# Kernel tuning notes

Hardware: AMD Instinct MI355X
Metric: run time of the kernel (lower is better)

The kernel has to match this reference:

```python
import jax, jax.numpy as jnp
from jax import lax
import numpy as np

LRELU_SLOPE = 0.1
DILATIONS = (1, 2, 4)
B, C, T = 8, 256, 8192


def pd_indexing(x, d, dilation):
    """Pitch-dependent past/future gather along time.
    x: (B, C, T); d: (B, 1, T) float dilation factors.
    Returns xP, xF: (B, C, T), zero where index is out of range.
    """
    b, c, t_len = x.shape
    t = jnp.arange(t_len, dtype=x.dtype)  # (T,)
    dil = d[:, 0, :] * dilation           # (B, T)
    idxP = jnp.round(t[None, :] - dil).astype(jnp.int32)  # (B, T)
    idxF = jnp.round(t[None, :] + dil).astype(jnp.int32)  # (B, T)
    validP = (idxP >= 0).astype(x.dtype)[:, None, :]        # (B,1,T)
    validF = (idxF < t_len).astype(x.dtype)[:, None, :]
    idxPc = jnp.broadcast_to(jnp.clip(idxP, 0, t_len - 1)[:, None, :], (b, c, t_len))
    idxFc = jnp.broadcast_to(jnp.clip(idxF, 0, t_len - 1)[:, None, :], (b, c, t_len))
    xP = jnp.take_along_axis(x, idxPc, axis=2) * validP
    xF = jnp.take_along_axis(x, idxFc, axis=2) * validF
    return xP, xF


def conv1x1(x, w, bias):
    # x: (B,C,T), w: (O,C), bias: (O,)
    return jnp.einsum('oc,bct->bot', w, x) + bias[None, :, None]


def conv3(x, w, bias):
    # x: (B,C,T), w: (O,C,3), padding=1
    y = lax.conv_general_dilated(x, w, window_strides=(1,), padding=[(1, 1)],
                                 dimension_numbers=('NCH', 'OIH', 'NCH'))
    return y + bias[None, :, None]


def setup_inputs() -> dict:
    key = jax.random.key(0)
    ks = jax.random.split(key, 8)
    x = jax.random.normal(ks[0], (B, C, T), dtype=jnp.float32)
    d = jax.random.uniform(ks[1], (B, 1, T), dtype=jnp.float32, minval=0.0, maxval=16.0)
    n = len(DILATIONS)
    s1 = 1.0 / np.sqrt(C)
    s3 = 1.0 / np.sqrt(3 * C)
    WC = jax.random.normal(ks[2], (n, C, C), dtype=jnp.float32) * s1
    WP = jax.random.normal(ks[3], (n, C, C), dtype=jnp.float32) * s1
    WF = jax.random.normal(ks[4], (n, C, C), dtype=jnp.float32) * s1
    WA = jax.random.normal(ks[5], (n, C, C, 3), dtype=jnp.float32) * s3
    bC = jnp.zeros((n, C), dtype=jnp.float32)
    bP = jnp.zeros((n, C), dtype=jnp.float32)
    bF = jnp.zeros((n, C), dtype=jnp.float32)
    bA = jnp.zeros((n, C), dtype=jnp.float32)
    return {"x": x, "d": d, "WC": WC, "bC": bC, "WP": WP, "bP": bP,
            "WF": WF, "bF": bF, "WA": WA, "bA": bA}


def reference(x, d, WC, bC, WP, bP, WF, bF, WA, bA):
    for i, dilation in enumerate(DILATIONS):
        xt = jax.nn.leaky_relu(x, LRELU_SLOPE)
        xP, xF = pd_indexing(xt, d, dilation)
        xt = conv1x1(xt, WC[i], bC[i]) + conv1x1(xP, WP[i], bP[i]) + conv1x1(xF, WF[i], bF[i])
        xt = jax.nn.leaky_relu(xt, LRELU_SLOPE)
        xt = conv3(xt, WA[i], bA[i])
        x = xt + x
    return x
```

## Files before the change

### kernel.cpp

```cpp
#include <hip/hip_runtime.h>
#include <hip/hip_bf16.h>
#include <cstddef>
#include <cstdint>

constexpr int Bn = 8, Cn = 256, Tn = 8192;
constexpr int NL = 3;
constexpr int Kc = 768;
constexpr float SLOPE = 0.1f;

typedef unsigned short u16;
using bf8   = __attribute__((ext_vector_type(8))) short;
using f32x4 = __attribute__((ext_vector_type(4))) float;

__device__ __forceinline__ float lrelu(float v) { return v > 0.f ? v : SLOPE * v; }
__device__ __forceinline__ u16 f2bf(float f) {
    __hip_bfloat16 h = __float2bfloat16(f);
    return *reinterpret_cast<u16*>(&h);
}

__device__ __forceinline__ void g2l16(const u16* g, u16* l) {
    __builtin_amdgcn_global_load_lds(
        (const __attribute__((address_space(1))) char*)g,
        (__attribute__((address_space(3))) char*)l, 16, 0, 0);
}

__device__ __forceinline__ void pipe_barrier() {
    __builtin_amdgcn_s_barrier();
    __builtin_amdgcn_sched_barrier(0);
}

__global__ __launch_bounds__(256)
void k_wprep(const float* __restrict__ WC, const float* __restrict__ WP,
             const float* __restrict__ WF, const float* __restrict__ WA,
             const float* __restrict__ bC, const float* __restrict__ bP,
             const float* __restrict__ bF,
             u16* __restrict__ Wcat, u16* __restrict__ WAp, float* __restrict__ bSum,
             u16* __restrict__ zrow)
{
    if (blockIdx.x == 0) zrow[threadIdx.x] = 0;
    const int n1 = NL * Cn * Kc;
    for (int i = blockIdx.x * blockDim.x + threadIdx.x; i < n1;
         i += gridDim.x * blockDim.x) {
        int c = i % Cn;
        int s = (i / Cn) % 3;
        int o = (i / (3 * Cn)) % Cn;
        int l = i / (3 * Cn * Cn);
        size_t src = ((size_t)l * Cn + o) * Cn + c;
        float wc = (s == 0) ? WC[src] : (s == 1) ? WP[src] : WF[src];
        Wcat[i] = f2bf(wc);
        WAp[i] = f2bf(WA[src * 3 + s]);
    }
    for (int i = blockIdx.x * blockDim.x + threadIdx.x; i < NL * Cn;
         i += gridDim.x * blockDim.x)
        bSum[i] = bC[i] + bP[i] + bF[i];
}

__global__ __launch_bounds__(256)
void k_prep(const float* __restrict__ x, u16* __restrict__ xT)
{
    __shared__ float s[64][65];
    const int b = blockIdx.z, c0 = blockIdx.y * 64, t0 = blockIdx.x * 64;
    const int tid = threadIdx.x;
    const float* xb = x + ((size_t)b * Cn + c0) * Tn + t0;

    int tt = tid & 63, c4 = tid >> 6;
    for (int cc = c4; cc < 64; cc += 4)
        s[cc][tt] = xb[(size_t)cc * Tn + tt];
    __syncthreads();

    int ccS = tid & 63, t4 = tid >> 6;
    u16* xTb = xT + ((size_t)b * Tn + t0) * Cn + c0;
    for (int t2 = t4; t2 < 64; t2 += 4)
        xTb[(size_t)t2 * Cn + ccS] = f2bf(lrelu(s[ccS][t2]));
}

__global__ __launch_bounds__(256, 2)
void k_gemm1(const u16* __restrict__ xT, const float* __restrict__ d,
             const u16* __restrict__ Wl, const float* __restrict__ bS,
             float dil, u16* __restrict__ zT, const u16* __restrict__ zrow)
{
    __shared__ u16 smem[8 * 4096];
    __shared__ int sRow[3][128];

    const int tid = threadIdx.x;
    const int b = blockIdx.z;
    const int fid = blockIdx.x;
    const int j = fid >> 3;
    const int o0 = (j & 1) * 128;
    const int t0 = ((fid & 7) * 8 + (j >> 1)) * 128;

    if (tid < 128) {
        int t = t0 + tid;
        float dv = d[(size_t)b * Tn + t] * dil;
        int ip = (int)rintf((float)t - dv);
        int iF = (int)rintf((float)t + dv);
        sRow[0][tid] = t;
        sRow[1][tid] = (ip >= 0) ? ip : -1;
        sRow[2][tid] = (iF < Tn) ? iF : -1;
    }
    __syncthreads();

    const int srow = tid >> 2;
    const int schunkL = (tid & 3) * 8;
    const int schunkG = ((tid & 3) ^ ((tid >> 3) & 3)) * 8;
    const u16* xTb = xT + (size_t)b * Tn * Cn;

    const u16 *pr0[3], *pr1[3];
    #pragma unroll
    for (int s = 0; s < 3; ++s) {
        int r0 = sRow[s][srow], r1 = sRow[s][srow + 64];
        pr0[s] = (r0 >= 0) ? (xTb + (size_t)r0 * Cn + schunkG) : (zrow + schunkG);
        pr1[s] = (r1 >= 0) ? (xTb + (size_t)r1 * Cn + schunkG) : (zrow + schunkG);
    }
    const u16* wbase = Wl + (size_t)(o0 + srow) * Kc + schunkG;

    const int lane = tid & 63, wv = tid >> 6;
    const int wm = (wv & 1) * 64;
    const int wn = (wv >> 1) * 64;
    const int lr = lane & 15, quad = lane >> 4;
    const int rchunk = (quad ^ ((lr >> 1) & 3)) * 8;

    const int ldsW = srow * 32 + schunkL;
    const int ldsW2 = (srow + 64) * 32 + schunkL;

    auto dma = [&](int kg, int bsel) {
        int seg = kg >> 3, kk = (kg & 7) * 32;
        u16* bx = smem + bsel * 4096;
        u16* bw = smem + 16384 + bsel * 4096;
        g2l16(wbase + seg * 256 + kk,                   bw + ldsW);
        g2l16(wbase + (size_t)64 * Kc + seg * 256 + kk, bw + ldsW2);
        g2l16(pr0[seg] + kk, bx + ldsW);
        g2l16(pr1[seg] + kk, bx + ldsW2);
    };

    f32x4 acc[4][4] = {};
    dma(0, 0); dma(1, 1);

    #pragma unroll
    for (int P = 0; P < 12; ++P) {
        const int k0 = 2 * P, k1 = 2 * P + 1;
        asm volatile("s_waitcnt vmcnt(0) lgkmcnt(0)" ::: "memory");
        pipe_barrier();
        if (P < 11) { dma(k0 + 2, (k0 + 2) & 3); dma(k1 + 2, (k1 + 2) & 3); }
        __builtin_amdgcn_sched_barrier(0);

        const u16* bX0 = smem + (k0 & 3) * 4096;
        const u16* bW0 = smem + 16384 + (k0 & 3) * 4096;
        const u16* bX1 = smem + (k1 & 3) * 4096;
        const u16* bW1 = smem + 16384 + (k1 & 3) * 4096;

        bf8 a0[4], g0[4], a1[4], g1[4];
        #pragma unroll
        for (int mi = 0; mi < 4; ++mi)
            a0[mi] = *(const bf8*)(bX0 + (wm + mi * 16 + lr) * 32 + rchunk);
        #pragma unroll
        for (int ni = 0; ni < 4; ++ni)
            g0[ni] = *(const bf8*)(bW0 + (wn + ni * 16 + lr) * 32 + rchunk);
        __builtin_amdgcn_sched_barrier(0);
        #pragma unroll
        for (int mi = 0; mi < 4; ++mi)
            a1[mi] = *(const bf8*)(bX1 + (wm + mi * 16 + lr) * 32 + rchunk);
        #pragma unroll
        for (int ni = 0; ni < 4; ++ni)
            g1[ni] = *(const bf8*)(bW1 + (wn + ni * 16 + lr) * 32 + rchunk);

        asm volatile("s_waitcnt lgkmcnt(8)" ::: "memory");
        __builtin_amdgcn_sched_barrier(0);
        __builtin_amdgcn_s_setprio(1);
        #pragma unroll
        for (int mi = 0; mi < 4; ++mi)
            #pragma unroll
            for (int ni = 0; ni < 4; ++ni)
                acc[mi][ni] = __builtin_amdgcn_mfma_f32_16x16x32_bf16(
                    a0[mi], g0[ni], acc[mi][ni], 0, 0, 0);
        __builtin_amdgcn_s_setprio(0);

        asm volatile("s_waitcnt lgkmcnt(0)" ::: "memory");
        __builtin_amdgcn_sched_barrier(0);
        __builtin_amdgcn_s_setprio(1);
        #pragma unroll
        for (int mi = 0; mi < 4; ++mi)
            #pragma unroll
            for (int ni = 0; ni < 4; ++ni)
                acc[mi][ni] = __builtin_amdgcn_mfma_f32_16x16x32_bf16(
                    a1[mi], g1[ni], acc[mi][ni], 0, 0, 0);
        __builtin_amdgcn_s_setprio(0);
    }

    float bias[4];
    #pragma unroll
    for (int ni = 0; ni < 4; ++ni) bias[ni] = bS[o0 + wn + ni * 16 + lr];
    u16* zTb = zT + (size_t)b * Tn * Cn;
    #pragma unroll
    for (int mi = 0; mi < 4; ++mi)
        #pragma unroll
        for (int r = 0; r < 4; ++r) {
            int t = t0 + wm + mi * 16 + quad * 4 + r;
            u16* row = zTb + (size_t)t * Cn + o0 + wn;
            #pragma unroll
            for (int ni = 0; ni < 4; ++ni)
                row[ni * 16 + lr] = f2bf(lrelu(acc[mi][ni][r] + bias[ni]));
        }
}

__global__ __launch_bounds__(256, 2)
void k_gemm2(const u16* __restrict__ zT, const u16* __restrict__ WAl,
             const float* __restrict__ bA, const float* __restrict__ xres,
             float* __restrict__ out, u16* __restrict__ xTn, int writeXT,
             const u16* __restrict__ zrow)
{
    __shared__ u16 smem[8 * 4096];

    const int tid = threadIdx.x;
    const int b = blockIdx.z;
    const int fid = blockIdx.x;
    const int j = fid >> 3;
    const int o0 = (j & 1) * 128;
    const int t0 = ((fid & 7) * 8 + (j >> 1)) * 128;

    const int srow = tid >> 2;
    const int schunkL = (tid & 3) * 8;
    const int schunkG = ((tid & 3) ^ ((tid >> 3) & 3)) * 8;
    const int lane = tid & 63, wv = tid >> 6;
    const int wo = (wv & 1) * 64;
    const int wt = (wv >> 1) * 64;
    const int lr = lane & 15, quad = lane >> 4;
    const int rchunk = (quad ^ ((lr >> 1) & 3)) * 8;

    const u16* zTb = zT + (size_t)b * Tn * Cn;
    const u16 *zr0[3], *zr1[3];
    #pragma unroll
    for (int tap = 0; tap < 3; ++tap) {
        int r0 = t0 + srow + tap - 1;
        int r1 = r0 + 64;
        zr0[tap] = (r0 >= 0 && r0 < Tn) ? (zTb + (size_t)r0 * Cn + schunkG)
                                        : (zrow + schunkG);
        zr1[tap] = (r1 >= 0 && r1 < Tn) ? (zTb + (size_t)r1 * Cn + schunkG)
                                        : (zrow + schunkG);
    }
    const u16* wbase = WAl + (size_t)(o0 + srow) * Kc + schunkG;

    const int ldsW = srow * 32 + schunkL;
    const int ldsW2 = (srow + 64) * 32 + schunkL;

    auto dma = [&](int kg, int bsel) {
        int tap = kg >> 3, kk = (kg & 7) * 32;
        u16* bz = smem + bsel * 4096;
        u16* bw = smem + 16384 + bsel * 4096;
        g2l16(wbase + tap * 256 + kk,                   bw + ldsW);
        g2l16(wbase + (size_t)64 * Kc + tap * 256 + kk, bw + ldsW2);
        g2l16(zr0[tap] + kk, bz + ldsW);
        g2l16(zr1[tap] + kk, bz + ldsW2);
    };

    f32x4 acc[4][4] = {};
    dma(0, 0); dma(1, 1);

    #pragma unroll
    for (int P = 0; P < 12; ++P) {
        const int k0 = 2 * P, k1 = 2 * P + 1;
        asm volatile("s_waitcnt vmcnt(0) lgkmcnt(0)" ::: "memory");
        pipe_barrier();
        if (P < 11) { dma(k0 + 2, (k0 + 2) & 3); dma(k1 + 2, (k1 + 2) & 3); }
        __builtin_amdgcn_sched_barrier(0);

        const u16* bZ0 = smem + (k0 & 3) * 4096;
        const u16* bW0 = smem + 16384 + (k0 & 3) * 4096;
        const u16* bZ1 = smem + (k1 & 3) * 4096;
        const u16* bW1 = smem + 16384 + (k1 & 3) * 4096;

        bf8 a0[4], g0[4], a1[4], g1[4];
        #pragma unroll
        for (int mi = 0; mi < 4; ++mi)
            a0[mi] = *(const bf8*)(bW0 + (wo + mi * 16 + lr) * 32 + rchunk);
        #pragma unroll
        for (int ni = 0; ni < 4; ++ni)
            g0[ni] = *(const bf8*)(bZ0 + (wt + ni * 16 + lr) * 32 + rchunk);
        __builtin_amdgcn_sched_barrier(0);
        #pragma unroll
        for (int mi = 0; mi < 4; ++mi)
            a1[mi] = *(const bf8*)(bW1 + (wo + mi * 16 + lr) * 32 + rchunk);
        #pragma unroll
        for (int ni = 0; ni < 4; ++ni)
            g1[ni] = *(const bf8*)(bZ1 + (wt + ni * 16 + lr) * 32 + rchunk);

        asm volatile("s_waitcnt lgkmcnt(8)" ::: "memory");
        __builtin_amdgcn_sched_barrier(0);
        __builtin_amdgcn_s_setprio(1);
        #pragma unroll
        for (int mi = 0; mi < 4; ++mi)
            #pragma unroll
            for (int ni = 0; ni < 4; ++ni)
                acc[mi][ni] = __builtin_amdgcn_mfma_f32_16x16x32_bf16(
                    a0[mi], g0[ni], acc[mi][ni], 0, 0, 0);
        __builtin_amdgcn_s_setprio(0);

        asm volatile("s_waitcnt lgkmcnt(0)" ::: "memory");
        __builtin_amdgcn_sched_barrier(0);
        __builtin_amdgcn_s_setprio(1);
        #pragma unroll
        for (int mi = 0; mi < 4; ++mi)
            #pragma unroll
            for (int ni = 0; ni < 4; ++ni)
                acc[mi][ni] = __builtin_amdgcn_mfma_f32_16x16x32_bf16(
                    a1[mi], g1[ni], acc[mi][ni], 0, 0, 0);
        __builtin_amdgcn_s_setprio(0);
    }

    float biasv[4][4];
    #pragma unroll
    for (int mi = 0; mi < 4; ++mi) {
        float4 bb = *(const float4*)(bA + o0 + wo + mi * 16 + quad * 4);
        biasv[mi][0] = bb.x; biasv[mi][1] = bb.y; biasv[mi][2] = bb.z; biasv[mi][3] = bb.w;
    }

    float xr0[16], xr1[16];
    ushort4 pkv[4][4];
    auto issue = [&](int ni, float* dst) {
        #pragma unroll
        for (int mi = 0; mi < 4; ++mi)
            #pragma unroll
            for (int r = 0; r < 4; ++r) {
                int o = o0 + wo + mi * 16 + quad * 4 + r;
                dst[mi * 4 + r] =
                    xres[((size_t)b * Cn + o) * Tn + t0 + wt + ni * 16 + lr];
            }
    };
    issue(0, xr0);
    #pragma unroll
    for (int ni = 0; ni < 4; ++ni) {
        float* cur = (ni & 1) ? xr1 : xr0;
        float* nxt = (ni & 1) ? xr0 : xr1;
        if (ni + 1 < 4) issue(ni + 1, nxt);
        #pragma unroll
        for (int mi = 0; mi < 4; ++mi) {
            ushort4 pk;
            #pragma unroll
            for (int r = 0; r < 4; ++r) {
                int o = o0 + wo + mi * 16 + quad * 4 + r;
                size_t idx = ((size_t)b * Cn + o) * Tn + t0 + wt + ni * 16 + lr;
                float v = acc[mi][ni][r] + biasv[mi][r] + cur[mi * 4 + r];
                out[idx] = v;
                ((u16*)&pk)[r] = f2bf(lrelu(v));
            }
            pkv[ni][mi] = pk;
        }
    }

    if (writeXT) {
        u16* strip = smem + wv * 1152;
        u16* xTb2 = xTn + (size_t)b * Tn * Cn;
        #pragma unroll
        for (int ni = 0; ni < 4; ++ni) {
            __syncthreads();
            #pragma unroll
            for (int mi = 0; mi < 4; ++mi)
                *(ushort4*)(strip + lr * 72 + mi * 16 + quad * 4) = pkv[ni][mi];
            __syncthreads();
            #pragma unroll
            for (int it = 0; it < 2; ++it) {
                int tt = (lane >> 3) + it * 8;
                uint4 vv = *(const uint4*)(strip + tt * 72 + (lane & 7) * 8);
                *(uint4*)(xTb2 + (size_t)(t0 + wt + ni * 16 + tt) * Cn
                          + o0 + wo + (lane & 7) * 8) = vv;
            }
        }
    }
}

extern "C" void kernel_launch(void* const* d_in, const int* in_sizes, int n_in,
                              void* d_out, int out_size, void* d_ws, size_t ws_size,
                              hipStream_t stream)
{
    const float* x  = (const float*)d_in[0];
    const float* d  = (const float*)d_in[1];
    const float* WC = (const float*)d_in[2];
    const float* bC = (const float*)d_in[3];
    const float* WP = (const float*)d_in[4];
    const float* bP = (const float*)d_in[5];
    const float* WF = (const float*)d_in[6];
    const float* bF = (const float*)d_in[7];
    const float* WA = (const float*)d_in[8];
    const float* bA = (const float*)d_in[9];
    float* out = (float*)d_out;

    char* ws = (char*)d_ws;
    u16*   xT   = (u16*)(ws);
    u16*   zT   = (u16*)(ws + (size_t)Bn * Tn * Cn * 2);
    u16*   Wcat = (u16*)(ws + (size_t)2 * Bn * Tn * Cn * 2);
    u16*   WAp  = Wcat + (size_t)NL * Cn * Kc;
    float* bSum = (float*)(WAp + (size_t)NL * Cn * Kc);
    u16*   zrow = (u16*)(bSum + NL * Cn);

    k_wprep<<<dim3(1024), dim3(256), 0, stream>>>(WC, WP, WF, WA, bC, bP, bF,
                                                  Wcat, WAp, bSum, zrow);

    dim3 gP(Tn / 64, Cn / 64, Bn);
    dim3 gG(128, 1, Bn);
    dim3 blk(256);

    k_prep<<<gP, blk, 0, stream>>>(x, xT);

    const float dils[NL] = {1.f, 2.f, 4.f};
    const float* xcur = x;
    for (int i = 0; i < NL; ++i) {
        k_gemm1<<<gG, blk, 0, stream>>>(xT, d,
                                        Wcat + (size_t)i * Cn * Kc,
                                        bSum + (size_t)i * Cn,
                                        dils[i], zT, zrow);
        k_gemm2<<<gG, blk, 0, stream>>>(zT,
                                        WAp + (size_t)i * Cn * Kc,
                                        bA + (size_t)i * Cn,
                                        xcur, out, xT, (i < NL - 1) ? 1 : 0,
                                        zrow);
        xcur = out;
    }
}
```

Before: 364.0 us.

## Loop each block over both output halves, coalesce zT stores, prefetch residual

Both GEMM kernels now assign one time tile per block and loop over the two 128-channel output halves inside the block, so the grid shrinks from 128 to 64 blocks per batch. The first GEMM now stages its bf16 epilogue through a per-wave LDS strip, so zT is written with 16-byte row stores instead of scattered 2-byte stores. The second GEMM loads half of the residual values before the main loop and drops the block-wide barriers from its per-wave transpose. In exchange, the two halves run back to back inside each block, and the smaller grid gives the GPU fewer blocks to spread across compute units.

```diff
diff --git a/kernel.cpp b/kernel.cpp
--- a/kernel.cpp
+++ b/kernel.cpp
@@ -85,9 +85,7 @@
     const int tid = threadIdx.x;
     const int b = blockIdx.z;
     const int fid = blockIdx.x;
-    const int j = fid >> 3;
-    const int o0 = (j & 1) * 128;
-    const int t0 = ((fid & 7) * 8 + (j >> 1)) * 128;
+    const int t0 = ((fid & 7) * 8 + (fid >> 3)) * 128;
 
     if (tid < 128) {
         int t = t0 + tid;
@@ -112,7 +110,6 @@
         pr0[s] = (r0 >= 0) ? (xTb + (size_t)r0 * Cn + schunkG) : (zrow + schunkG);
         pr1[s] = (r1 >= 0) ? (xTb + (size_t)r1 * Cn + schunkG) : (zrow + schunkG);
     }
-    const u16* wbase = Wl + (size_t)(o0 + srow) * Kc + schunkG;
 
     const int lane = tid & 63, wv = tid >> 6;
     const int wm = (wv & 1) * 64;
@@ -122,85 +119,102 @@
 
     const int ldsW = srow * 32 + schunkL;
     const int ldsW2 = (srow + 64) * 32 + schunkL;
-
-    auto dma = [&](int kg, int bsel) {
-        int seg = kg >> 3, kk = (kg & 7) * 32;
-        u16* bx = smem + bsel * 4096;
-        u16* bw = smem + 16384 + bsel * 4096;
-        g2l16(wbase + seg * 256 + kk,                   bw + ldsW);
-        g2l16(wbase + (size_t)64 * Kc + seg * 256 + kk, bw + ldsW2);
-        g2l16(pr0[seg] + kk, bx + ldsW);
-        g2l16(pr1[seg] + kk, bx + ldsW2);
-    };
-
-    f32x4 acc[4][4] = {};
-    dma(0, 0); dma(1, 1);
-
-    #pragma unroll
-    for (int P = 0; P < 12; ++P) {
-        const int k0 = 2 * P, k1 = 2 * P + 1;
-        asm volatile("s_waitcnt vmcnt(0) lgkmcnt(0)" ::: "memory");
-        pipe_barrier();
-        if (P < 11) { dma(k0 + 2, (k0 + 2) & 3); dma(k1 + 2, (k1 + 2) & 3); }
-        __builtin_amdgcn_sched_barrier(0);
-
-        const u16* bX0 = smem + (k0 & 3) * 4096;
-        const u16* bW0 = smem + 16384 + (k0 & 3) * 4096;
-        const u16* bX1 = smem + (k1 & 3) * 4096;
-        const u16* bW1 = smem + 16384 + (k1 & 3) * 4096;
-
-        bf8 a0[4], g0[4], a1[4], g1[4];
-        #pragma unroll
-        for (int mi = 0; mi < 4; ++mi)
-            a0[mi] = *(const bf8*)(bX0 + (wm + mi * 16 + lr) * 32 + rchunk);
-        #pragma unroll
-        for (int ni = 0; ni < 4; ++ni)
-            g0[ni] = *(const bf8*)(bW0 + (wn + ni * 16 + lr) * 32 + rchunk);
-        __builtin_amdgcn_sched_barrier(0);
-        #pragma unroll
-        for (int mi = 0; mi < 4; ++mi)
-            a1[mi] = *(const bf8*)(bX1 + (wm + mi * 16 + lr) * 32 + rchunk);
-        #pragma unroll
-        for (int ni = 0; ni < 4; ++ni)
-            g1[ni] = *(const bf8*)(bW1 + (wn + ni * 16 + lr) * 32 + rchunk);
-
-        asm volatile("s_waitcnt lgkmcnt(8)" ::: "memory");
-        __builtin_amdgcn_sched_barrier(0);
-        __builtin_amdgcn_s_setprio(1);
-        #pragma unroll
-        for (int mi = 0; mi < 4; ++mi)
+    u16* zTb = zT + (size_t)b * Tn * Cn;
+
+    #pragma unroll 1
+    for (int h = 0; h < 2; ++h) {
+        const int o0 = h * 128;
+        if (h) __syncthreads();
+
+        const u16* wbase = Wl + (size_t)(o0 + srow) * Kc + schunkG;
+        auto dma = [&](int kg, int bsel) {
+            int seg = kg >> 3, kk = (kg & 7) * 32;
+            u16* bx = smem + bsel * 4096;
+            u16* bw = smem + 16384 + bsel * 4096;
+            g2l16(wbase + seg * 256 + kk,                   bw + ldsW);
+            g2l16(wbase + (size_t)64 * Kc + seg * 256 + kk, bw + ldsW2);
+            g2l16(pr0[seg] + kk, bx + ldsW);
+            g2l16(pr1[seg] + kk, bx + ldsW2);
+        };
+
+        float bias[4];
+        #pragma unroll
+        for (int ni = 0; ni < 4; ++ni) bias[ni] = bS[o0 + wn + ni * 16 + lr];
+
+        f32x4 acc[4][4] = {};
+        dma(0, 0); dma(1, 1);
+
+        #pragma unroll
+        for (int P = 0; P < 12; ++P) {
+            const int k0 = 2 * P, k1 = 2 * P + 1;
+            asm volatile("s_waitcnt vmcnt(0) lgkmcnt(0)" ::: "memory");
+            pipe_barrier();
+            if (P < 11) { dma(k0 + 2, (k0 + 2) & 3); dma(k1 + 2, (k1 + 2) & 3); }
+            __builtin_amdgcn_sched_barrier(0);
+
+            const u16* bX0 = smem + (k0 & 3) * 4096;
+            const u16* bW0 = smem + 16384 + (k0 & 3) * 4096;
+            const u16* bX1 = smem + (k1 & 3) * 4096;
+            const u16* bW1 = smem + 16384 + (k1 & 3) * 4096;
+
+            bf8 a0[4], g0[4], a1[4], g1[4];
+            #pragma unroll
+            for (int mi = 0; mi < 4; ++mi)
+                a0[mi] = *(const bf8*)(bX0 + (wm + mi * 16 + lr) * 32 + rchunk);
             #pragma unroll
             for (int ni = 0; ni < 4; ++ni)
-                acc[mi][ni] = __builtin_amdgcn_mfma_f32_16x16x32_bf16(
-                    a0[mi], g0[ni], acc[mi][ni], 0, 0, 0);
-        __builtin_amdgcn_s_setprio(0);
-
-        asm volatile("s_waitcnt lgkmcnt(0)" ::: "memory");
-        __builtin_amdgcn_sched_barrier(0);
-        __builtin_amdgcn_s_setprio(1);
-        #pragma unroll
-        for (int mi = 0; mi < 4; ++mi)
+                g0[ni] = *(const bf8*)(bW0 + (wn + ni * 16 + lr) * 32 + rchunk);
+            __builtin_amdgcn_sched_barrier(0);
+            #pragma unroll
+            for (int mi = 0; mi < 4; ++mi)
+                a1[mi] = *(const bf8*)(bX1 + (wm + mi * 16 + lr) * 32 + rchunk);
             #pragma unroll
             for (int ni = 0; ni < 4; ++ni)
-                acc[mi][ni] = __builtin_amdgcn_mfma_f32_16x16x32_bf16(
-                    a1[mi], g1[ni], acc[mi][ni], 0, 0, 0);
-        __builtin_amdgcn_s_setprio(0);
-    }
-
-    float bias[4];
-    #pragma unroll
-    for (int ni = 0; ni < 4; ++ni) bias[ni] = bS[o0 + wn + ni * 16 + lr];
-    u16* zTb = zT + (size_t)b * Tn * Cn;
-    #pragma unroll
-    for (int mi = 0; mi < 4; ++mi)
-        #pragma unroll
-        for (int r = 0; r < 4; ++r) {
-            int t = t0 + wm + mi * 16 + quad * 4 + r;
-            u16* row = zTb + (size_t)t * Cn + o0 + wn;
-            #pragma unroll
-            for (int ni = 0; ni < 4; ++ni)
-                row[ni * 16 + lr] = f2bf(lrelu(acc[mi][ni][r] + bias[ni]));
-        }
+                g1[ni] = *(const bf8*)(bW1 + (wn + ni * 16 + lr) * 32 + rchunk);
+
+            asm volatile("s_waitcnt lgkmcnt(8)" ::: "memory");
+            __builtin_amdgcn_sched_barrier(0);
+            __builtin_amdgcn_s_setprio(1);
+            #pragma unroll
+            for (int mi = 0; mi < 4; ++mi)
+                #pragma unroll
+                for (int ni = 0; ni < 4; ++ni)
+                    acc[mi][ni] = __builtin_amdgcn_mfma_f32_16x16x32_bf16(
+                        a0[mi], g0[ni], acc[mi][ni], 0, 0, 0);
+            __builtin_amdgcn_s_setprio(0);
+
+            asm volatile("s_waitcnt lgkmcnt(0)" ::: "memory");
+            __builtin_amdgcn_sched_barrier(0);
+            __builtin_amdgcn_s_setprio(1);
+            #pragma unroll
+            for (int mi = 0; mi < 4; ++mi)
+                #pragma unroll
+                for (int ni = 0; ni < 4; ++ni)
+                    acc[mi][ni] = __builtin_amdgcn_mfma_f32_16x16x32_bf16(
+                        a1[mi], g1[ni], acc[mi][ni], 0, 0, 0);
+            __builtin_amdgcn_s_setprio(0);
+        }
+
+        u16* strip = smem + wv * 1152;
+        #pragma unroll
+        for (int mi = 0; mi < 4; ++mi) {
+            #pragma unroll
+            for (int r = 0; r < 4; ++r) {
+                int tq = quad * 4 + r;
+                #pragma unroll
+                for (int ni = 0; ni < 4; ++ni)
+                    strip[tq * 72 + ni * 16 + lr] =
+                        f2bf(lrelu(acc[mi][ni][r] + bias[ni]));
+            }
+            #pragma unroll
+            for (int it = 0; it < 2; ++it) {
+                int tt = (lane >> 3) + it * 8;
+                uint4 vv = *(const uint4*)(strip + tt * 72 + (lane & 7) * 8);
+                *(uint4*)(zTb + (size_t)(t0 + wm + mi * 16 + tt) * Cn
+                          + o0 + wn + (lane & 7) * 8) = vv;
+            }
+        }
+    }
 }
 
 __global__ __launch_bounds__(256, 2)
@@ -214,9 +228,7 @@
     const int tid = threadIdx.x;
     const int b = blockIdx.z;
     const int fid = blockIdx.x;
-    const int j = fid >> 3;
-    const int o0 = (j & 1) * 128;
-    const int t0 = ((fid & 7) * 8 + (j >> 1)) * 128;
+    const int t0 = ((fid & 7) * 8 + (fid >> 3)) * 128;
 
     const int srow = tid >> 2;
     const int schunkL = (tid & 3) * 8;
@@ -238,131 +250,145 @@
         zr1[tap] = (r1 >= 0 && r1 < Tn) ? (zTb + (size_t)r1 * Cn + schunkG)
                                         : (zrow + schunkG);
     }
-    const u16* wbase = WAl + (size_t)(o0 + srow) * Kc + schunkG;
 
     const int ldsW = srow * 32 + schunkL;
     const int ldsW2 = (srow + 64) * 32 + schunkL;
-
-    auto dma = [&](int kg, int bsel) {
-        int tap = kg >> 3, kk = (kg & 7) * 32;
-        u16* bz = smem + bsel * 4096;
-        u16* bw = smem + 16384 + bsel * 4096;
-        g2l16(wbase + tap * 256 + kk,                   bw + ldsW);
-        g2l16(wbase + (size_t)64 * Kc + tap * 256 + kk, bw + ldsW2);
-        g2l16(zr0[tap] + kk, bz + ldsW);
-        g2l16(zr1[tap] + kk, bz + ldsW2);
-    };
-
-    f32x4 acc[4][4] = {};
-    dma(0, 0); dma(1, 1);
-
-    #pragma unroll
-    for (int P = 0; P < 12; ++P) {
-        const int k0 = 2 * P, k1 = 2 * P + 1;
-        asm volatile("s_waitcnt vmcnt(0) lgkmcnt(0)" ::: "memory");
-        pipe_barrier();
-        if (P < 11) { dma(k0 + 2, (k0 + 2) & 3); dma(k1 + 2, (k1 + 2) & 3); }
-        __builtin_amdgcn_sched_barrier(0);
-
-        const u16* bZ0 = smem + (k0 & 3) * 4096;
-        const u16* bW0 = smem + 16384 + (k0 & 3) * 4096;
-        const u16* bZ1 = smem + (k1 & 3) * 4096;
-        const u16* bW1 = smem + 16384 + (k1 & 3) * 4096;
-
-        bf8 a0[4], g0[4], a1[4], g1[4];
-        #pragma unroll
-        for (int mi = 0; mi < 4; ++mi)
-            a0[mi] = *(const bf8*)(bW0 + (wo + mi * 16 + lr) * 32 + rchunk);
-        #pragma unroll
-        for (int ni = 0; ni < 4; ++ni)
-            g0[ni] = *(const bf8*)(bZ0 + (wt + ni * 16 + lr) * 32 + rchunk);
-        __builtin_amdgcn_sched_barrier(0);
-        #pragma unroll
-        for (int mi = 0; mi < 4; ++mi)
-            a1[mi] = *(const bf8*)(bW1 + (wo + mi * 16 + lr) * 32 + rchunk);
-        #pragma unroll
-        for (int ni = 0; ni < 4; ++ni)
-            g1[ni] = *(const bf8*)(bZ1 + (wt + ni * 16 + lr) * 32 + rchunk);
-
-        asm volatile("s_waitcnt lgkmcnt(8)" ::: "memory");
-        __builtin_amdgcn_sched_barrier(0);
-        __builtin_amdgcn_s_setprio(1);
-        #pragma unroll
-        for (int mi = 0; mi < 4; ++mi)
+    u16* xTb2 = xTn + (size_t)b * Tn * Cn;
+
+    #pragma unroll 1
+    for (int h = 0; h < 2; ++h) {
+        const int o0 = h * 128;
+        if (h) __syncthreads();
+
+        const u16* wbase = WAl + (size_t)(o0 + srow) * Kc + schunkG;
+        auto dma = [&](int kg, int bsel) {
+            int tap = kg >> 3, kk = (kg & 7) * 32;
+            u16* bz = smem + bsel * 4096;
+            u16* bw = smem + 16384 + bsel * 4096;
+            g2l16(wbase + tap * 256 + kk,                   bw + ldsW);
+            g2l16(wbase + (size_t)64 * Kc + tap * 256 + kk, bw + ldsW2);
+            g2l16(zr0[tap] + kk, bz + ldsW);
+            g2l16(zr1[tap] + kk, bz + ldsW2);
+        };
+
+        float biasv[4][4];
+        #pragma unroll
+        for (int mi = 0; mi < 4; ++mi) {
+            float4 bb = *(const float4*)(bA + o0 + wo + mi * 16 + quad * 4);
+            biasv[mi][0] = bb.x; biasv[mi][1] = bb.y;
+            biasv[mi][2] = bb.z; biasv[mi][3] = bb.w;
+        }
+        float xr01[32];
+        #pragma unroll
+        for (int g = 0; g < 2; ++g)
+            #pragma unroll
+            for (int mi = 0; mi < 4; ++mi)
+                #pragma unroll
+                for (int r = 0; r < 4; ++r) {
+                    int o = o0 + wo + mi * 16 + quad * 4 + r;
+                    xr01[g * 16 + mi * 4 + r] =
+                        xres[((size_t)b * Cn + o) * Tn + t0 + wt + g * 16 + lr];
+                }
+
+        f32x4 acc[4][4] = {};
+        dma(0, 0); dma(1, 1);
+
+        #pragma unroll
+        for (int P = 0; P < 12; ++P) {
+            const int k0 = 2 * P, k1 = 2 * P + 1;
+            asm volatile("s_waitcnt vmcnt(0) lgkmcnt(0)" ::: "memory");
+            pipe_barrier();
+            if (P < 11) { dma(k0 + 2, (k0 + 2) & 3); dma(k1 + 2, (k1 + 2) & 3); }
+            __builtin_amdgcn_sched_barrier(0);
+
+            const u16* bZ0 = smem + (k0 & 3) * 4096;
+            const u16* bW0 = smem + 16384 + (k0 & 3) * 4096;
+            const u16* bZ1 = smem + (k1 & 3) * 4096;
+            const u16* bW1 = smem + 16384 + (k1 & 3) * 4096;
+
+            bf8 a0[4], g0[4], a1[4], g1[4];
+            #pragma unroll
+            for (int mi = 0; mi < 4; ++mi)
+                a0[mi] = *(const bf8*)(bW0 + (wo + mi * 16 + lr) * 32 + rchunk);
             #pragma unroll
             for (int ni = 0; ni < 4; ++ni)
-                acc[mi][ni] = __builtin_amdgcn_mfma_f32_16x16x32_bf16(
-                    a0[mi], g0[ni], acc[mi][ni], 0, 0, 0);
-        __builtin_amdgcn_s_setprio(0);
-
-        asm volatile("s_waitcnt lgkmcnt(0)" ::: "memory");
-        __builtin_amdgcn_sched_barrier(0);
-        __builtin_amdgcn_s_setprio(1);
-        #pragma unroll
-        for (int mi = 0; mi < 4; ++mi)
+                g0[ni] = *(const bf8*)(bZ0 + (wt + ni * 16 + lr) * 32 + rchunk);
+            __builtin_amdgcn_sched_barrier(0);
+            #pragma unroll
+            for (int mi = 0; mi < 4; ++mi)
+                a1[mi] = *(const bf8*)(bW1 + (wo + mi * 16 + lr) * 32 + rchunk);
             #pragma unroll
             for (int ni = 0; ni < 4; ++ni)
-                acc[mi][ni] = __builtin_amdgcn_mfma_f32_16x16x32_bf16(
-                    a1[mi], g1[ni], acc[mi][ni], 0, 0, 0);
-        __builtin_amdgcn_s_setprio(0);
-    }
-
-    float biasv[4][4];
-    #pragma unroll
-    for (int mi = 0; mi < 4; ++mi) {
-        float4 bb = *(const float4*)(bA + o0 + wo + mi * 16 + quad * 4);
-        biasv[mi][0] = bb.x; biasv[mi][1] = bb.y; biasv[mi][2] = bb.z; biasv[mi][3] = bb.w;
-    }
-
-    float xr0[16], xr1[16];
-    ushort4 pkv[4][4];
-    auto issue = [&](int ni, float* dst) {
-        #pragma unroll
-        for (int mi = 0; mi < 4; ++mi)
-            #pragma unroll
-            for (int r = 0; r < 4; ++r) {
-                int o = o0 + wo + mi * 16 + quad * 4 + r;
-                dst[mi * 4 + r] =
-                    xres[((size_t)b * Cn + o) * Tn + t0 + wt + ni * 16 + lr];
+                g1[ni] = *(const bf8*)(bZ1 + (wt + ni * 16 + lr) * 32 + rchunk);
+
+            asm volatile("s_waitcnt lgkmcnt(8)" ::: "memory");
+            __builtin_amdgcn_sched_barrier(0);
+            __builtin_amdgcn_s_setprio(1);
+            #pragma unroll
+            for (int mi = 0; mi < 4; ++mi)
+                #pragma unroll
+                for (int ni = 0; ni < 4; ++ni)
+                    acc[mi][ni] = __builtin_amdgcn_mfma_f32_16x16x32_bf16(
+                        a0[mi], g0[ni], acc[mi][ni], 0, 0, 0);
+            __builtin_amdgcn_s_setprio(0);
+
+            asm volatile("s_waitcnt lgkmcnt(0)" ::: "memory");
+            __builtin_amdgcn_sched_barrier(0);
+            __builtin_amdgcn_s_setprio(1);
+            #pragma unroll
+            for (int mi = 0; mi < 4; ++mi)
+                #pragma unroll
+                for (int ni = 0; ni < 4; ++ni)
+                    acc[mi][ni] = __builtin_amdgcn_mfma_f32_16x16x32_bf16(
+                        a1[mi], g1[ni], acc[mi][ni], 0, 0, 0);
+            __builtin_amdgcn_s_setprio(0);
+        }
+
+        float xr23[32];
+        #pragma unroll
+        for (int g = 0; g < 2; ++g)
+            #pragma unroll
+            for (int mi = 0; mi < 4; ++mi)
+                #pragma unroll
+                for (int r = 0; r < 4; ++r) {
+                    int o = o0 + wo + mi * 16 + quad * 4 + r;
+                    xr23[g * 16 + mi * 4 + r] =
+                        xres[((size_t)b * Cn + o) * Tn + t0 + wt + (g + 2) * 16 + lr];
+                }
+
+        ushort4 pkv[4][4];
+        #pragma unroll
+        for (int ni = 0; ni < 4; ++ni) {
+            const float* cur = (ni < 2) ? (xr01 + ni * 16) : (xr23 + (ni - 2) * 16);
+            #pragma unroll
+            for (int mi = 0; mi < 4; ++mi) {
+                ushort4 pk;
+                #pragma unroll
+                for (int r = 0; r < 4; ++r) {
+                    int o = o0 + wo + mi * 16 + quad * 4 + r;
+                    size_t idx = ((size_t)b * Cn + o) * Tn + t0 + wt + ni * 16 + lr;
+                    float v = acc[mi][ni][r] + biasv[mi][r] + cur[mi * 4 + r];
+                    out[idx] = v;
+                    ((u16*)&pk)[r] = f2bf(lrelu(v));
+                }
+                pkv[ni][mi] = pk;
             }
-    };
-    issue(0, xr0);
-    #pragma unroll
-    for (int ni = 0; ni < 4; ++ni) {
-        float* cur = (ni & 1) ? xr1 : xr0;
-        float* nxt = (ni & 1) ? xr0 : xr1;
-        if (ni + 1 < 4) issue(ni + 1, nxt);
-        #pragma unroll
-        for (int mi = 0; mi < 4; ++mi) {
-            ushort4 pk;
-            #pragma unroll
-            for (int r = 0; r < 4; ++r) {
-                int o = o0 + wo + mi * 16 + quad * 4 + r;
-                size_t idx = ((size_t)b * Cn + o) * Tn + t0 + wt + ni * 16 + lr;
-                float v = acc[mi][ni][r] + biasv[mi][r] + cur[mi * 4 + r];
-                out[idx] = v;
-                ((u16*)&pk)[r] = f2bf(lrelu(v));
-            }
-            pkv[ni][mi] = pk;
-        }
-    }
-
-    if (writeXT) {
-        u16* strip = smem + wv * 1152;
-        u16* xTb2 = xTn + (size_t)b * Tn * Cn;
-        #pragma unroll
-        for (int ni = 0; ni < 4; ++ni) {
-            __syncthreads();
-            #pragma unroll
-            for (int mi = 0; mi < 4; ++mi)
-                *(ushort4*)(strip + lr * 72 + mi * 16 + quad * 4) = pkv[ni][mi];
-            __syncthreads();
-            #pragma unroll
-            for (int it = 0; it < 2; ++it) {
-                int tt = (lane >> 3) + it * 8;
-                uint4 vv = *(const uint4*)(strip + tt * 72 + (lane & 7) * 8);
-                *(uint4*)(xTb2 + (size_t)(t0 + wt + ni * 16 + tt) * Cn
-                          + o0 + wo + (lane & 7) * 8) = vv;
+        }
+
+        if (writeXT) {
+            u16* strip = smem + wv * 1152;
+            #pragma unroll
+            for (int ni = 0; ni < 4; ++ni) {
+                #pragma unroll
+                for (int mi = 0; mi < 4; ++mi)
+                    *(ushort4*)(strip + lr * 72 + mi * 16 + quad * 4) = pkv[ni][mi];
+                #pragma unroll
+                for (int it = 0; it < 2; ++it) {
+                    int tt = (lane >> 3) + it * 8;
+                    uint4 vv = *(const uint4*)(strip + tt * 72 + (lane & 7) * 8);
+                    *(uint4*)(xTb2 + (size_t)(t0 + wt + ni * 16 + tt) * Cn
+                              + o0 + wo + (lane & 7) * 8) = vv;
+                }
             }
         }
     }
@@ -396,7 +422,7 @@
                                                   Wcat, WAp, bSum, zrow);
 
     dim3 gP(Tn / 64, Cn / 64, Bn);
-    dim3 gG(128, 1, Bn);
+    dim3 gG(64, 1, Bn);
     dim3 blk(256);
 
     k_prep<<<gP, blk, 0, stream>>>(x, xT);
```

New measurement: 745.3 us. +104.8%, slower.
